# Performance work log

Hardware: AMD Instinct MI355X
Metric: run time of the kernel (lower is better)

Reference implementation:

```python
import jax, jax.numpy as jnp
import numpy as np

INF = jnp.float32(np.inf)
LAMBDA_VAL = 1.0
NUM_CLASSES = 10

def setup_inputs() -> dict:
    key = jax.random.key(0)
    k1, k2, k3 = jax.random.split(key, 3)
    N, P, D = 65536, 2048, 64
    x = jax.random.normal(k1, (N, D), dtype=jnp.float32)
    y = jax.random.randint(k2, (N,), 0, NUM_CLASSES)
    prototypes = jax.random.normal(k3, (P, D), dtype=jnp.float32)
    prototype_labels = jnp.arange(P) % NUM_CLASSES
    return {"x": x, "y": y, "prototypes": prototypes, "prototype_labels": prototype_labels}

def _cdist(x, p):
    # Euclidean pairwise distances via the gemm expansion (matches torch.cdist default
    x2 = jnp.sum(x * x, axis=1, keepdims=True)          # [N, 1]
    p2 = jnp.sum(p * p, axis=1)                          # [P]
    sq = x2 + p2[None, :] - 2.0 * (x @ p.T)              # [N, P]
    return jnp.sqrt(jnp.maximum(sq, 0.0))

def reference(x, y, prototypes, prototype_labels):
    distances = _cdist(x, prototypes)                    # [N, P]
    same = prototype_labels[None, :] == y[:, None]       # [N, P] bool
    pos = jnp.min(jnp.where(same, distances, INF), axis=1)   # [N]
    neg = jnp.min(jnp.where(~same, distances, INF), axis=1)  # [N]
    mu = (pos - neg) / (pos + neg)
    loss = jnp.mean(jax.nn.sigmoid(LAMBDA_VAL * mu))
    return loss
```

## Files before the change

### kernel.cpp

```cpp
#include <hip/hip_runtime.h>
#include <math.h>

#define NROWS  65536
#define NPROTO 2048
#define DDIM   64
#define NCLS   10

#define NPROTO_PAD 2560
#define CHUNK_BYTES 8448
#define NCHUNKS     40
#define CHUNKS_PER_WAVE 20

typedef __attribute__((ext_vector_type(8))) short bf16x8;
typedef __attribute__((ext_vector_type(4))) float f32x4;
typedef __attribute__((ext_vector_type(4))) unsigned int u32x4;

__device__ inline unsigned int f2bf(float f) {
    unsigned int u = __float_as_uint(f);
    return (u + 0x7FFFu + ((u >> 16) & 1u)) >> 16;
}

__global__ __launch_bounds__(256) void convert_kernel(
        const float* __restrict__ protos, char* __restrict__ wsB,
        float* __restrict__ out) {
    int t = blockIdx.x * 256 + threadIdx.x;
    int s = t >> 3, jj = t & 7;
    int L = s >> 8, j = s & 255;
    int cnt = (L < 8) ? 205 : 204;
    bool real = (j < cnt);
    float v[8] = {0.f, 0.f, 0.f, 0.f, 0.f, 0.f, 0.f, 0.f};
    if (real) {
        const float* src = protos + (L + 10 * j) * DDIM + jj * 8;
        float4 a = *(const float4*)src;
        float4 b = *(const float4*)(src + 4);
        v[0] = a.x; v[1] = a.y; v[2] = a.z; v[3] = a.w;
        v[4] = b.x; v[5] = b.y; v[6] = b.z; v[7] = b.w;
    }
    float ss = 0.f;
#pragma unroll
    for (int i = 0; i < 8; i++) ss = fmaf(v[i], v[i], ss);
    ss += __shfl_xor(ss, 1, 64);
    ss += __shfl_xor(ss, 2, 64);
    ss += __shfl_xor(ss, 4, 64);
    unsigned int w[4];
#pragma unroll
    for (int i = 0; i < 4; i++) {
        unsigned int lo = f2bf(-2.f * v[2 * i]);
        unsigned int hi = f2bf(-2.f * v[2 * i + 1]);
        w[i] = lo | (hi << 16);
    }
    int c = s >> 6, r = s & 63;
    size_t off = (size_t)c * CHUNK_BYTES + (size_t)(r * 8 + (jj ^ (r & 7))) * 16;
    *(u32x4*)(wsB + off) = (u32x4){w[0], w[1], w[2], w[3]};
    if (jj == 0)
        *(float*)(wsB + (size_t)c * CHUNK_BYTES + 8192 + r * 4) =
            real ? ss : __builtin_inff();
    if (t == 0) out[0] = 0.f;
}

__global__ __launch_bounds__(128, 2) void glvq_kernel(
        const float* __restrict__ x, const int* __restrict__ y,
        const char* __restrict__ wsB, float* __restrict__ out) {
    __shared__ __align__(16) char ldsBuf[2][2][CHUNK_BYTES];
    __shared__ float2 sPN[128];
    __shared__ float  sX2[64];

    const int tid  = threadIdx.x;
    const int wave = tid >> 6;
    const int lane = tid & 63;
    const int quad = lane >> 4;
    const int l15  = lane & 15;
    const int rowBase = blockIdx.x * 64;
    const float CINF = __builtin_inff();

    sPN[wave * 64 + lane] = make_float2(CINF, CINF);

    bf16x8 afrag[4][2];
    float x2r[4];
#pragma unroll
    for (int m = 0; m < 4; m++) {
        const float* xr = x + (size_t)(rowBase + m * 16 + l15) * DDIM;
        float part = 0.f;
#pragma unroll
        for (int k = 0; k < 2; k++) {
            const float* sp = xr + k * 32 + quad * 8;
            float4 u0 = *(const float4*)sp;
            float4 u1 = *(const float4*)(sp + 4);
            float vv[8] = {u0.x, u0.y, u0.z, u0.w, u1.x, u1.y, u1.z, u1.w};
#pragma unroll
            for (int i = 0; i < 8; i++) part = fmaf(vv[i], vv[i], part);
            bf16x8 af;
#pragma unroll
            for (int i = 0; i < 8; i++) af[i] = (short)f2bf(vv[i]);
            afrag[m][k] = af;
        }
        part += __shfl_xor(part, 16, 64);
        part += __shfl_xor(part, 32, 64);
        x2r[m] = part;
    }
    if (wave == 0 && quad == 0) {
#pragma unroll
        for (int m = 0; m < 4; m++) sX2[m * 16 + l15] = x2r[m];
    }

    int ypack[4];
#pragma unroll
    for (int m = 0; m < 4; m++) {
        int4 yq = *(const int4*)(y + rowBase + m * 16 + quad * 4);
        ypack[m] = (yq.x & 0xFF) | ((yq.y & 0xFF) << 8) |
                   ((yq.z & 0xFF) << 16) | (yq.w << 24);
    }

    float mMin[4][4];
#pragma unroll
    for (int m = 0; m < 4; m++)
#pragma unroll
        for (int r = 0; r < 4; r++) mMin[m][r] = CINF;

    char* b0 = ldsBuf[wave][0];
    char* b1 = ldsBuf[wave][1];
    const int chunk0 = wave * CHUNKS_PER_WAVE;

    auto stageChunk = [&](int g, char* buf) {
        const char* s = wsB + (size_t)g * CHUNK_BYTES;
#pragma unroll
        for (int i = 0; i < 8; i++)
            __builtin_amdgcn_global_load_lds(
                (const __attribute__((address_space(1))) void*)(s + i * 1024 + lane * 16),
                (__attribute__((address_space(3))) void*)(buf + i * 1024),
                16, 0, 0);
        __builtin_amdgcn_global_load_lds(
            (const __attribute__((address_space(1))) void*)(s + 8192 + lane * 4),
            (__attribute__((address_space(3))) void*)(buf + 8192),
            4, 0, 0);
    };

    auto computeChunk = [&](const char* buf) {
#pragma unroll
        for (int fg = 0; fg < 2; fg++) {
            const int fA = fg * 2, fB = fg * 2 + 1;
            float p2a = *(const float*)(buf + 8192 + (fA * 16 + l15) * 4);
            float p2b = *(const float*)(buf + 8192 + (fB * 16 + l15) * 4);
            f32x4 acc[4][2];
#pragma unroll
            for (int m = 0; m < 4; m++) {
                acc[m][0] = (f32x4){p2a, p2a, p2a, p2a};
                acc[m][1] = (f32x4){p2b, p2b, p2b, p2b};
            }
#pragma unroll
            for (int k = 0; k < 2; k++) {
                bf16x8 bA = *(const bf16x8*)(buf +
                    ((fA * 16 + l15) * 8 + ((k * 4 + quad) ^ (l15 & 7))) * 16);
                bf16x8 bB = *(const bf16x8*)(buf +
                    ((fB * 16 + l15) * 8 + ((k * 4 + quad) ^ (l15 & 7))) * 16);
#pragma unroll
                for (int m = 0; m < 4; m++) {
                    acc[m][0] = __builtin_amdgcn_mfma_f32_16x16x32_bf16(
                        afrag[m][k], bA, acc[m][0], 0, 0, 0);
                    acc[m][1] = __builtin_amdgcn_mfma_f32_16x16x32_bf16(
                        afrag[m][k], bB, acc[m][1], 0, 0, 0);
                }
            }
#pragma unroll
            for (int m = 0; m < 4; m++)
#pragma unroll
                for (int r = 0; r < 4; r++)
                    mMin[m][r] = fminf(fminf(acc[m][0][r], acc[m][1][r]),
                                       mMin[m][r]);
        }
    };

    auto mergeGroup = [&](int L) {
#pragma unroll
        for (int m = 0; m < 4; m++)
#pragma unroll
            for (int r = 0; r < 4; r++) {
                float v = mMin[m][r];
                v = fminf(v, __shfl_xor(v, 1, 64));
                v = fminf(v, __shfl_xor(v, 2, 64));
                v = fminf(v, __shfl_xor(v, 4, 64));
                v = fminf(v, __shfl_xor(v, 8, 64));
                if (l15 == 0) {
                    int yb = (ypack[m] >> (8 * r)) & 0xFF;
                    int idx = wave * 64 + m * 16 + quad * 4 + r;
                    float2 pn = sPN[idx];
                    if (yb == L) pn.x = fminf(pn.x, v);
                    else         pn.y = fminf(pn.y, v);
                    sPN[idx] = pn;
                }
                mMin[m][r] = CINF;
            }
    };

    stageChunk(chunk0 + 0, b0);
    stageChunk(chunk0 + 1, b1);
#pragma unroll 1
    for (int c = 0; c < CHUNKS_PER_WAVE; c += 2) {
        asm volatile("s_waitcnt vmcnt(9)" ::: "memory");
        computeChunk(b0);
        asm volatile("s_waitcnt lgkmcnt(0)" ::: "memory");
        if (c + 2 < CHUNKS_PER_WAVE) {
            stageChunk(chunk0 + c + 2, b0);
            asm volatile("s_waitcnt vmcnt(9)" ::: "memory");
        } else {
            asm volatile("s_waitcnt vmcnt(0)" ::: "memory");
        }
        computeChunk(b1);
        asm volatile("s_waitcnt lgkmcnt(0)" ::: "memory");
        if (c + 2 < CHUNKS_PER_WAVE)
            stageChunk(chunk0 + c + 3, b1);
        int absc = chunk0 + c + 1;
        if ((absc & 3) == 3)
            mergeGroup(absc >> 2);
    }

    __syncthreads();

    if (wave == 0) {
        float2 a = sPN[lane], b = sPN[64 + lane];
        float mp = fminf(a.x, b.x);
        float mn = fminf(a.y, b.y);
        float x2v = sX2[lane];
        float sp = sqrtf(fmaxf(x2v + mp, 0.f));
        float sn = sqrtf(fmaxf(x2v + mn, 0.f));
        float mu = (sp - sn) / (sp + sn);
        float lsum = 1.f / (1.f + __expf(-mu));
#pragma unroll
        for (int o = 1; o <= 32; o <<= 1)
            lsum += __shfl_xor(lsum, o, 64);
        if (lane == 0)
            atomicAdd(out, lsum * (1.f / (float)NROWS));
    }
}

extern "C" void kernel_launch(void* const* d_in, const int* in_sizes, int n_in,
                              void* d_out, int out_size, void* d_ws, size_t ws_size,
                              hipStream_t stream) {
    const float* x      = (const float*)d_in[0];
    const int*   y      = (const int*)d_in[1];
    const float* protos = (const float*)d_in[2];
    float* out = (float*)d_out;
    char*  wsB = (char*)d_ws;

    convert_kernel<<<NPROTO_PAD * 8 / 256, 256, 0, stream>>>(protos, wsB, out);
    glvq_kernel<<<NROWS / 64, 128, 0, stream>>>(x, y, wsB, out);
}
```

Baseline: 113.6 us.

## Split prototype work across grid y-dimension and write per-class mins to workspace

Each block now holds 8 prototype chunks (two class groups) resident in LDS. A 2D grid splits the prototype set into 5 pieces, so every block loads its prototype image once and skips the per-wave double-buffered streaming loop. Per-class minima are reduced with DPP row-rotate and written as fp16 to a workspace plane. A separate combine kernel then selects pos/neg per label and computes the sigmoid loss, and a separate x2 kernel computes row norms. This trades the in-loop staging and pipelining for more parallelism, extra launches, re-reading x once per piece, and fp16 rounding of the minimum distances.

```diff
diff --git a/kernel.cpp b/kernel.cpp
--- a/kernel.cpp
+++ b/kernel.cpp
@@ -8,8 +8,11 @@
 
 #define NPROTO_PAD 2560
 #define CHUNK_BYTES 8448
-#define NCHUNKS     40
-#define CHUNKS_PER_WAVE 20
+
+#define WS_IMG_BYTES   (40 * CHUNK_BYTES)
+#define WS_MINS_OFF    WS_IMG_BYTES
+#define WS_MINS_BYTES  (NCLS * NROWS * 2)
+#define WS_X2_OFF      (WS_MINS_OFF + WS_MINS_BYTES)
 
 typedef __attribute__((ext_vector_type(8))) short bf16x8;
 typedef __attribute__((ext_vector_type(4))) float f32x4;
@@ -18,6 +21,12 @@
 __device__ inline unsigned int f2bf(float f) {
     unsigned int u = __float_as_uint(f);
     return (u + 0x7FFFu + ((u >> 16) & 1u)) >> 16;
+}
+
+template <int CTRL>
+__device__ inline float rorMin(float v) {
+    int t = __builtin_amdgcn_update_dpp(0, __float_as_int(v), CTRL, 0xF, 0xF, false);
+    return fminf(v, __int_as_float(t));
 }
 
 __global__ __launch_bounds__(256) void convert_kernel(
@@ -58,179 +67,166 @@
     if (t == 0) out[0] = 0.f;
 }
 
-__global__ __launch_bounds__(128, 2) void glvq_kernel(
-        const float* __restrict__ x, const int* __restrict__ y,
-        const char* __restrict__ wsB, float* __restrict__ out) {
-    __shared__ __align__(16) char ldsBuf[2][2][CHUNK_BYTES];
-    __shared__ float2 sPN[128];
-    __shared__ float  sX2[64];
+__global__ __launch_bounds__(256) void x2_kernel(const float* __restrict__ x,
+                                                 float* __restrict__ wsX2) {
+    int t = blockIdx.x * 256 + threadIdx.x;
+    int row = t >> 4, j = t & 15;
+    float4 v = ((const float4*)(x + (size_t)row * DDIM))[j];
+    float s = v.x * v.x;
+    s = fmaf(v.y, v.y, s);
+    s = fmaf(v.z, v.z, s);
+    s = fmaf(v.w, v.w, s);
+    s += __shfl_xor(s, 1, 64);
+    s += __shfl_xor(s, 2, 64);
+    s += __shfl_xor(s, 4, 64);
+    s += __shfl_xor(s, 8, 64);
+    if (j == 0) wsX2[row] = s;
+}
+
+__global__ __launch_bounds__(512, 4) void glvq_main(
+        const float* __restrict__ x, const char* __restrict__ wsB,
+        _Float16* __restrict__ wsMins) {
+    __shared__ __align__(16) char ldsImg[8][CHUNK_BYTES];
 
     const int tid  = threadIdx.x;
     const int wave = tid >> 6;
     const int lane = tid & 63;
     const int quad = lane >> 4;
     const int l15  = lane & 15;
-    const int rowBase = blockIdx.x * 64;
+    const int piece = blockIdx.y;
     const float CINF = __builtin_inff();
 
-    sPN[wave * 64 + lane] = make_float2(CINF, CINF);
-
+    {
+        const char* src = wsB + (size_t)(piece * 8 + wave) * CHUNK_BYTES;
+        char* dst = ldsImg[wave];
+#pragma unroll
+        for (int i = 0; i < 8; i++)
+            __builtin_amdgcn_global_load_lds(
+                (const __attribute__((address_space(1))) void*)(src + i * 1024 + lane * 16),
+                (__attribute__((address_space(3))) void*)(dst + i * 1024),
+                16, 0, 0);
+        __builtin_amdgcn_global_load_lds(
+            (const __attribute__((address_space(1))) void*)(src + 8192 + lane * 4),
+            (__attribute__((address_space(3))) void*)(dst + 8192),
+            4, 0, 0);
+    }
+    asm volatile("s_waitcnt vmcnt(0)" ::: "memory");
+    __syncthreads();
+
+    const int rowBase = (blockIdx.x * 8 + wave) * 64;
     bf16x8 afrag[4][2];
-    float x2r[4];
 #pragma unroll
     for (int m = 0; m < 4; m++) {
         const float* xr = x + (size_t)(rowBase + m * 16 + l15) * DDIM;
-        float part = 0.f;
 #pragma unroll
         for (int k = 0; k < 2; k++) {
             const float* sp = xr + k * 32 + quad * 8;
             float4 u0 = *(const float4*)sp;
             float4 u1 = *(const float4*)(sp + 4);
             float vv[8] = {u0.x, u0.y, u0.z, u0.w, u1.x, u1.y, u1.z, u1.w};
-#pragma unroll
-            for (int i = 0; i < 8; i++) part = fmaf(vv[i], vv[i], part);
             bf16x8 af;
 #pragma unroll
             for (int i = 0; i < 8; i++) af[i] = (short)f2bf(vv[i]);
             afrag[m][k] = af;
         }
-        part += __shfl_xor(part, 16, 64);
-        part += __shfl_xor(part, 32, 64);
-        x2r[m] = part;
-    }
-    if (wave == 0 && quad == 0) {
-#pragma unroll
-        for (int m = 0; m < 4; m++) sX2[m * 16 + l15] = x2r[m];
-    }
-
-    int ypack[4];
-#pragma unroll
-    for (int m = 0; m < 4; m++) {
-        int4 yq = *(const int4*)(y + rowBase + m * 16 + quad * 4);
-        ypack[m] = (yq.x & 0xFF) | ((yq.y & 0xFF) << 8) |
-                   ((yq.z & 0xFF) << 16) | (yq.w << 24);
-    }
-
-    float mMin[4][4];
-#pragma unroll
-    for (int m = 0; m < 4; m++)
-#pragma unroll
-        for (int r = 0; r < 4; r++) mMin[m][r] = CINF;
-
-    char* b0 = ldsBuf[wave][0];
-    char* b1 = ldsBuf[wave][1];
-    const int chunk0 = wave * CHUNKS_PER_WAVE;
-
-    auto stageChunk = [&](int g, char* buf) {
-        const char* s = wsB + (size_t)g * CHUNK_BYTES;
-#pragma unroll
-        for (int i = 0; i < 8; i++)
-            __builtin_amdgcn_global_load_lds(
-                (const __attribute__((address_space(1))) void*)(s + i * 1024 + lane * 16),
-                (__attribute__((address_space(3))) void*)(buf + i * 1024),
-                16, 0, 0);
-        __builtin_amdgcn_global_load_lds(
-            (const __attribute__((address_space(1))) void*)(s + 8192 + lane * 4),
-            (__attribute__((address_space(3))) void*)(buf + 8192),
-            4, 0, 0);
-    };
-
-    auto computeChunk = [&](const char* buf) {
-#pragma unroll
-        for (int fg = 0; fg < 2; fg++) {
-            const int fA = fg * 2, fB = fg * 2 + 1;
-            float p2a = *(const float*)(buf + 8192 + (fA * 16 + l15) * 4);
-            float p2b = *(const float*)(buf + 8192 + (fB * 16 + l15) * 4);
-            f32x4 acc[4][2];
-#pragma unroll
-            for (int m = 0; m < 4; m++) {
-                acc[m][0] = (f32x4){p2a, p2a, p2a, p2a};
-                acc[m][1] = (f32x4){p2b, p2b, p2b, p2b};
+    }
+
+#pragma unroll
+    for (int ph = 0; ph < 2; ph++) {
+        float mMin[4][4];
+#pragma unroll
+        for (int m = 0; m < 4; m++)
+#pragma unroll
+            for (int r = 0; r < 4; r++) mMin[m][r] = CINF;
+
+#pragma unroll
+        for (int c = 0; c < 4; c++) {
+            const char* buf = ldsImg[ph * 4 + c];
+#pragma unroll
+            for (int fg = 0; fg < 2; fg++) {
+                const int fA = fg * 2, fB = fg * 2 + 1;
+                float p2a = *(const float*)(buf + 8192 + (fA * 16 + l15) * 4);
+                float p2b = *(const float*)(buf + 8192 + (fB * 16 + l15) * 4);
+                f32x4 acc[4][2];
+#pragma unroll
+                for (int m = 0; m < 4; m++) {
+                    acc[m][0] = (f32x4){p2a, p2a, p2a, p2a};
+                    acc[m][1] = (f32x4){p2b, p2b, p2b, p2b};
+                }
+#pragma unroll
+                for (int k = 0; k < 2; k++) {
+                    bf16x8 bA = *(const bf16x8*)(buf +
+                        ((fA * 16 + l15) * 8 + ((k * 4 + quad) ^ (l15 & 7))) * 16);
+                    bf16x8 bB = *(const bf16x8*)(buf +
+                        ((fB * 16 + l15) * 8 + ((k * 4 + quad) ^ (l15 & 7))) * 16);
+#pragma unroll
+                    for (int m = 0; m < 4; m++) {
+                        acc[m][0] = __builtin_amdgcn_mfma_f32_16x16x32_bf16(
+                            afrag[m][k], bA, acc[m][0], 0, 0, 0);
+                        acc[m][1] = __builtin_amdgcn_mfma_f32_16x16x32_bf16(
+                            afrag[m][k], bB, acc[m][1], 0, 0, 0);
+                    }
+                }
+#pragma unroll
+                for (int m = 0; m < 4; m++)
+#pragma unroll
+                    for (int r = 0; r < 4; r++)
+                        mMin[m][r] = fminf(fminf(acc[m][0][r], acc[m][1][r]),
+                                           mMin[m][r]);
             }
-#pragma unroll
-            for (int k = 0; k < 2; k++) {
-                bf16x8 bA = *(const bf16x8*)(buf +
-                    ((fA * 16 + l15) * 8 + ((k * 4 + quad) ^ (l15 & 7))) * 16);
-                bf16x8 bB = *(const bf16x8*)(buf +
-                    ((fB * 16 + l15) * 8 + ((k * 4 + quad) ^ (l15 & 7))) * 16);
-#pragma unroll
-                for (int m = 0; m < 4; m++) {
-                    acc[m][0] = __builtin_amdgcn_mfma_f32_16x16x32_bf16(
-                        afrag[m][k], bA, acc[m][0], 0, 0, 0);
-                    acc[m][1] = __builtin_amdgcn_mfma_f32_16x16x32_bf16(
-                        afrag[m][k], bB, acc[m][1], 0, 0, 0);
-                }
-            }
-#pragma unroll
-            for (int m = 0; m < 4; m++)
-#pragma unroll
-                for (int r = 0; r < 4; r++)
-                    mMin[m][r] = fminf(fminf(acc[m][0][r], acc[m][1][r]),
-                                       mMin[m][r]);
         }
-    };
-
-    auto mergeGroup = [&](int L) {
+
 #pragma unroll
         for (int m = 0; m < 4; m++)
 #pragma unroll
             for (int r = 0; r < 4; r++) {
                 float v = mMin[m][r];
-                v = fminf(v, __shfl_xor(v, 1, 64));
-                v = fminf(v, __shfl_xor(v, 2, 64));
-                v = fminf(v, __shfl_xor(v, 4, 64));
-                v = fminf(v, __shfl_xor(v, 8, 64));
-                if (l15 == 0) {
-                    int yb = (ypack[m] >> (8 * r)) & 0xFF;
-                    int idx = wave * 64 + m * 16 + quad * 4 + r;
-                    float2 pn = sPN[idx];
-                    if (yb == L) pn.x = fminf(pn.x, v);
-                    else         pn.y = fminf(pn.y, v);
-                    sPN[idx] = pn;
-                }
-                mMin[m][r] = CINF;
+                v = rorMin<0x128>(v);
+                v = rorMin<0x124>(v);
+                v = rorMin<0x122>(v);
+                v = rorMin<0x121>(v);
+                mMin[m][r] = v;
             }
-    };
-
-    stageChunk(chunk0 + 0, b0);
-    stageChunk(chunk0 + 1, b1);
-#pragma unroll 1
-    for (int c = 0; c < CHUNKS_PER_WAVE; c += 2) {
-        asm volatile("s_waitcnt vmcnt(9)" ::: "memory");
-        computeChunk(b0);
-        asm volatile("s_waitcnt lgkmcnt(0)" ::: "memory");
-        if (c + 2 < CHUNKS_PER_WAVE) {
-            stageChunk(chunk0 + c + 2, b0);
-            asm volatile("s_waitcnt vmcnt(9)" ::: "memory");
-        } else {
-            asm volatile("s_waitcnt vmcnt(0)" ::: "memory");
+
+        if (l15 == 0) {
+            _Float16* plane = wsMins + (size_t)(piece * 2 + ph) * NROWS + rowBase;
+#pragma unroll
+            for (int m = 0; m < 4; m++)
+#pragma unroll
+                for (int r = 0; r < 4; r++)
+                    plane[m * 16 + quad * 4 + r] = (_Float16)mMin[m][r];
         }
-        computeChunk(b1);
-        asm volatile("s_waitcnt lgkmcnt(0)" ::: "memory");
-        if (c + 2 < CHUNKS_PER_WAVE)
-            stageChunk(chunk0 + c + 3, b1);
-        int absc = chunk0 + c + 1;
-        if ((absc & 3) == 3)
-            mergeGroup(absc >> 2);
-    }
-
+    }
+}
+
+__global__ __launch_bounds__(256) void combine_kernel(
+        const int* __restrict__ y, const _Float16* __restrict__ wsMins,
+        const float* __restrict__ wsX2, float* __restrict__ out) {
+    int row = blockIdx.x * 256 + threadIdx.x;
+    int yr = y[row];
+    float pos = 0.f, neg = __builtin_inff();
+#pragma unroll
+    for (int L = 0; L < NCLS; L++) {
+        float d = (float)wsMins[(size_t)L * NROWS + row];
+        bool isPos = (L == yr);
+        pos = isPos ? d : pos;
+        neg = isPos ? neg : fminf(neg, d);
+    }
+    float x2v = wsX2[row];
+    float sp = sqrtf(fmaxf(x2v + pos, 0.f));
+    float sn = sqrtf(fmaxf(x2v + neg, 0.f));
+    float mu = (sp - sn) / (sp + sn);
+    float s = 1.f / (1.f + __expf(-mu));
+
+    __shared__ float red[256];
+    red[threadIdx.x] = s;
     __syncthreads();
-
-    if (wave == 0) {
-        float2 a = sPN[lane], b = sPN[64 + lane];
-        float mp = fminf(a.x, b.x);
-        float mn = fminf(a.y, b.y);
-        float x2v = sX2[lane];
-        float sp = sqrtf(fmaxf(x2v + mp, 0.f));
-        float sn = sqrtf(fmaxf(x2v + mn, 0.f));
-        float mu = (sp - sn) / (sp + sn);
-        float lsum = 1.f / (1.f + __expf(-mu));
-#pragma unroll
-        for (int o = 1; o <= 32; o <<= 1)
-            lsum += __shfl_xor(lsum, o, 64);
-        if (lane == 0)
-            atomicAdd(out, lsum * (1.f / (float)NROWS));
-    }
+#pragma unroll
+    for (int off = 128; off > 0; off >>= 1) {
+        if (threadIdx.x < off) red[threadIdx.x] += red[threadIdx.x + off];
+        __syncthreads();
+    }
+    if (threadIdx.x == 0) atomicAdd(out, red[0] * (1.f / (float)NROWS));
 }
 
 extern "C" void kernel_launch(void* const* d_in, const int* in_sizes, int n_in,
@@ -240,8 +236,13 @@
     const int*   y      = (const int*)d_in[1];
     const float* protos = (const float*)d_in[2];
     float* out = (float*)d_out;
-    char*  wsB = (char*)d_ws;
+
+    char*      wsB    = (char*)d_ws;
+    _Float16*  wsMins = (_Float16*)((char*)d_ws + WS_MINS_OFF);
+    float*     wsX2   = (float*)((char*)d_ws + WS_X2_OFF);
 
     convert_kernel<<<NPROTO_PAD * 8 / 256, 256, 0, stream>>>(protos, wsB, out);
-    glvq_kernel<<<NROWS / 64, 128, 0, stream>>>(x, y, wsB, out);
-}
+    x2_kernel<<<NROWS * 16 / 256, 256, 0, stream>>>(x, wsX2);
+    glvq_main<<<dim3(128, 5), 512, 0, stream>>>(x, wsB, wsMins);
+    combine_kernel<<<NROWS / 256, 256, 0, stream>>>(y, wsMins, wsX2, out);
+}
```

Result: faster. 108.6 us (-4.4%).
